# Optimization experiments

Hardware: AMD Instinct MI355X
Metric: run time of the kernel (lower is better)

## Reference

```python
import jax, jax.numpy as jnp
import numpy as np

BS, N, F, R, OUT = 8, 512, 512, 16, 512
ALPHA = 0.2

def setup_inputs() -> dict:
    key = jax.random.key(0)
    ks = jax.random.split(key, 16)
    w = lambda k, shp: (jax.random.normal(k, shp, dtype=jnp.float32) * 0.05)
    return {
        'x_ori': jax.random.normal(ks[0], (BS, N, F), dtype=jnp.float32),
        'x': jax.random.normal(ks[1], (BS, N, F), dtype=jnp.float32),
        'c': jax.random.normal(ks[2], (BS, 1, F), dtype=jnp.float32),
        'adj': jax.random.randint(ks[3], (BS, N, N, R), 0, 2, dtype=jnp.int32),
        'Wfc': w(ks[4], (F, F)),
        'Wdc': w(ks[5], (F, F)),
        'Wqv': w(ks[6], (2 * F, F)),
        'Wkv': w(ks[7], (2 * F, F)),
        'Wqc': w(ks[8], (F, F)),
        'Wkc': w(ks[9], (F, F)),
        'Wa': w(ks[10], (2 * F, R)),
        'Wu': w(ks[11], (2 * F, OUT)),
    }

def reference(x_ori, x, c, adj, Wfc, Wdc, Wqv, Wkv, Wqc, Wkc, Wa, Wu):
    # relation-context modulation vector m: [bs,1,F]
    m = jnp.matmul(jax.nn.elu(jnp.matmul(c, Wfc)), Wdc)
    nodes = jnp.concatenate([x, x_ori], axis=2)          # [bs,N,2F]
    xq = jnp.matmul(nodes, Wqv) * jnp.matmul(m, Wqc)     # [bs,N,F]
    xk = jnp.matmul(nodes, Wkv) * jnp.matmul(m, Wkc)     # [bs,N,F]
    # scores[b,i,j,r] = leakyrelu(xq_i . Wa[:F,r] + xk_j . Wa[F:,r])
    # (equivalent to cat([xq_i,xk_j]) @ Wa without materializing [bs,N,N,2F])
    sq = jnp.matmul(xq, Wa[:F])                          # [bs,N,R]
    sk = jnp.matmul(xk, Wa[F:])                          # [bs,N,R]
    scores = jax.nn.leaky_relu(sq[:, :, None, :] + sk[:, None, :, :], ALPHA)
    adj_f = adj.astype(scores.dtype)                     # [bs,N,N,R]
    s = jnp.sum(scores * adj_f, axis=3)                  # [bs,N,N]
    mask = jnp.sum(adj_f, axis=3) > 0
    attn = jax.nn.softmax(jnp.where(mask, s, jnp.float32(-9e15)), axis=2)
    new_x = jnp.matmul(attn, x)                          # [bs,N,F]
    return jnp.matmul(jnp.concatenate([x, new_x], axis=2), Wu)
```

## Files before the change

### kernel.cpp

```cpp
#include <hip/hip_runtime.h>
#include <hip/hip_bf16.h>
#include <cstddef>
#include <cstdint>

static constexpr int BSZ  = 8;
static constexpr int NN   = 512;
static constexpr int FF   = 512;
static constexpr int RR   = 16;
static constexpr int TWOF = 1024;

typedef __attribute__((ext_vector_type(8))) short short8;
typedef __attribute__((ext_vector_type(4))) float f32x4;

__device__ __forceinline__ ushort bf16_bits(float v) {
    union { __hip_bfloat16 h; ushort u; } cvt;
    cvt.h = __float2bfloat16(v);
    return cvt.u;
}

static constexpr size_t OFF_TB     = 0;
static constexpr size_t OFF_MB     = 16384;
static constexpr size_t OFF_MQ     = 32768;
static constexpr size_t OFF_MK     = 49152;
static constexpr size_t OFF_SQ     = 65536;
static constexpr size_t OFF_SK     = 327680;
static constexpr size_t OFF_WQET   = 589824;
static constexpr size_t OFF_WKET   = 851968;
static constexpr size_t OFF_XBF    = 5308416;
static constexpr size_t OFF_XTBF   = 9502720;
static constexpr size_t OFF_XORIBF = 13697024;
static constexpr size_t OFF_NEWXBF = 17891328;
static constexpr size_t OFF_WUT    = 22085632;
static constexpr size_t OFF_MASK   = 23134208;

__global__ __launch_bounds__(256) void k_prep(
    const float* __restrict__ x_ori, const float* __restrict__ x,
    const float* __restrict__ c, const float* __restrict__ Wfc,
    const float* __restrict__ Wu, const int* __restrict__ adj,
    ushort* __restrict__ xori_bf, ushort* __restrict__ x_bf,
    ushort* __restrict__ xT_bf, ushort* __restrict__ WuT,
    float* __restrict__ tb, ushort* __restrict__ masks)
{
    int blk = blockIdx.x;
    int t = threadIdx.x;
    if (blk < 1024) {
        int idx = blk * 256 + t;
        float4 a = ((const float4*)x_ori)[idx * 2];
        float4 b = ((const float4*)x_ori)[idx * 2 + 1];
        uint4 s;
        s.x = (uint)bf16_bits(a.x) | ((uint)bf16_bits(a.y) << 16);
        s.y = (uint)bf16_bits(a.z) | ((uint)bf16_bits(a.w) << 16);
        s.z = (uint)bf16_bits(b.x) | ((uint)bf16_bits(b.y) << 16);
        s.w = (uint)bf16_bits(b.z) | ((uint)bf16_bits(b.w) << 16);
        ((uint4*)xori_bf)[idx] = s;
    } else if (blk < 3072) {
        __shared__ float tile[32][33];
        int bb = blk - 1024;
        int f0 = (bb & 15) * 32, i0 = ((bb >> 4) & 15) * 32, b = bb >> 8;
        int c2 = (t & 15) * 2, r = t >> 4;
#pragma unroll
        for (int rr = 0; rr < 32; rr += 16) {
            int i = i0 + r + rr;
            const float* xp = &x[((size_t)b * NN + i) * FF + f0 + c2];
            float v0 = xp[0], v1 = xp[1];
            tile[r + rr][c2] = v0;
            tile[r + rr][c2 + 1] = v1;
            *(uint*)&x_bf[((size_t)b * NN + i) * FF + f0 + c2] =
                (uint)bf16_bits(v0) | ((uint)bf16_bits(v1) << 16);
        }
        __syncthreads();
#pragma unroll
        for (int ff = 0; ff < 32; ff += 16) {
            int f = f0 + r + ff;
            *(uint*)&xT_bf[((size_t)b * FF + f) * NN + i0 + c2] =
                (uint)bf16_bits(tile[c2][r + ff]) |
                ((uint)bf16_bits(tile[c2 + 1][r + ff]) << 16);
        }
    } else if (blk < 3584) {
        __shared__ float tile2[32][33];
        int bb = blk - 3072;
        int f0 = (bb & 31) * 32, o0 = (bb >> 5) * 32;
        int cc = t & 31, r0 = t >> 5;
#pragma unroll
        for (int rr = 0; rr < 32; rr += 8)
            tile2[r0 + rr][cc] = Wu[(size_t)(f0 + r0 + rr) * FF + o0 + cc];
        __syncthreads();
#pragma unroll
        for (int rr = 0; rr < 32; rr += 8)
            WuT[(size_t)(o0 + r0 + rr) * TWOF + f0 + cc] = bf16_bits(tile2[cc][r0 + rr]);
    } else if (blk < 3712) {
        __shared__ float red1[8][32];
        int bb = blk - 3584;
        int b = bb >> 4, f0 = (bb & 15) * 32;
        int f = t & 31, kq = t >> 5;
        const float* vb = c + (size_t)b * FF;
        float acc = 0.f;
        int ks = kq * 64;
#pragma unroll 8
        for (int k = ks; k < ks + 64; ++k)
            acc = fmaf(vb[k], Wfc[(size_t)k * FF + f0 + f], acc);
        red1[kq][f] = acc;
        __syncthreads();
        if (kq == 0) {
            acc += red1[1][f] + red1[2][f] + red1[3][f] + red1[4][f] +
                   red1[5][f] + red1[6][f] + red1[7][f];
            tb[(size_t)b * FF + f0 + f] = (acc > 0.f) ? acc : expm1f(acc);
        }
    } else {
        int idx = (blk - 3712) * 256 + t;
        const int4* ap = (const int4*)adj + (size_t)idx * 4;
        int4 a0 = ap[0], a1 = ap[1], a2 = ap[2], a3 = ap[3];
        uint m = 0;
        m |= (uint)a0.x;       m |= (uint)a0.y << 1;
        m |= (uint)a0.z << 2;  m |= (uint)a0.w << 3;
        m |= (uint)a1.x << 4;  m |= (uint)a1.y << 5;
        m |= (uint)a1.z << 6;  m |= (uint)a1.w << 7;
        m |= (uint)a2.x << 8;  m |= (uint)a2.y << 9;
        m |= (uint)a2.z << 10; m |= (uint)a2.w << 11;
        m |= (uint)a3.x << 12; m |= (uint)a3.y << 13;
        m |= (uint)a3.z << 14; m |= (uint)a3.w << 15;
        uint hi = (uint)__shfl_down((int)m, 1, 64);
        if (!(t & 1))
            ((uint*)masks)[idx >> 1] = m | (hi << 16);
    }
}

__global__ __launch_bounds__(256) void k_matvec(const float* __restrict__ vin,
                                                const float* __restrict__ W,
                                                float* __restrict__ vout) {
    __shared__ float red[8][32];
    int b = blockIdx.y;
    int f0 = blockIdx.x * 32;
    int t = threadIdx.x;
    int f = t & 31, kq = t >> 5;
    const float* vb = vin + (size_t)b * FF;
    float acc = 0.f;
    int ks = kq * 64;
#pragma unroll 8
    for (int k = ks; k < ks + 64; ++k)
        acc = fmaf(vb[k], W[(size_t)k * FF + f0 + f], acc);
    red[kq][f] = acc;
    __syncthreads();
    if (kq == 0) {
        acc += red[1][f] + red[2][f] + red[3][f] + red[4][f] +
               red[5][f] + red[6][f] + red[7][f];
        vout[(size_t)b * FF + f0 + f] = acc;
    }
}

__global__ __launch_bounds__(256) void k_mqk(const float* __restrict__ m,
                                             const float* __restrict__ Wqc,
                                             const float* __restrict__ Wkc,
                                             float* __restrict__ mq,
                                             float* __restrict__ mk) {
    __shared__ float redq[8][32];
    __shared__ float redk[8][32];
    int b = blockIdx.y;
    int f0 = blockIdx.x * 32;
    int t = threadIdx.x;
    int f = t & 31, kq = t >> 5;
    const float* mb = m + (size_t)b * FF;
    float aq = 0.f, ak = 0.f;
    int ks = kq * 64;
#pragma unroll 8
    for (int k = ks; k < ks + 64; ++k) {
        float mv = mb[k];
        aq = fmaf(mv, Wqc[(size_t)k * FF + f0 + f], aq);
        ak = fmaf(mv, Wkc[(size_t)k * FF + f0 + f], ak);
    }
    redq[kq][f] = aq;
    redk[kq][f] = ak;
    __syncthreads();
    if (kq == 0) {
        aq += redq[1][f] + redq[2][f] + redq[3][f] + redq[4][f] +
              redq[5][f] + redq[6][f] + redq[7][f];
        ak += redk[1][f] + redk[2][f] + redk[3][f] + redk[4][f] +
              redk[5][f] + redk[6][f] + redk[7][f];
        mq[(size_t)b * FF + f0 + f] = aq;
        mk[(size_t)b * FF + f0 + f] = ak;
    }
}

__global__ __launch_bounds__(256) void k_weff(const float* __restrict__ Wqv,
                                              const float* __restrict__ Wkv,
                                              const float* __restrict__ Wa,
                                              const float* __restrict__ mqv,
                                              const float* __restrict__ mkv,
                                              ushort* __restrict__ WqEt,
                                              ushort* __restrict__ WkEt) {
    int z = blockIdx.z;
    const float* W = z ? Wkv : Wqv;
    const float* mvec = z ? mkv : mqv;
    ushort* WeffT = z ? WkEt : WqEt;
    int waRowOff = z ? FF : 0;

    __shared__ float4 wa4[FF * 4];
    int tid = threadIdx.x;
    int b = blockIdx.y;
    const float* mv = mvec + (size_t)b * FF;
#pragma unroll
    for (int qq = 0; qq < 8; ++qq) {
        int idx = tid + qq * 256;
        int f = idx >> 2, rq = idx & 3;
        float4 w = *reinterpret_cast<const float4*>(Wa + (size_t)(waRowOff + f) * RR + rq * 4);
        float s = mv[f];
        float4 o;
        o.x = w.x * s; o.y = w.y * s; o.z = w.z * s; o.w = w.w * s;
        wa4[idx] = o;
    }
    __syncthreads();
    int k_l = tid >> 2, r4 = tid & 3;
    int k = blockIdx.x * 64 + k_l;
    const float4* Wrow4 = reinterpret_cast<const float4*>(W + (size_t)k * FF);
    float4 acc = {0.f, 0.f, 0.f, 0.f};
#pragma unroll 4
    for (int f4 = 0; f4 < FF / 4; ++f4) {
        float4 w = Wrow4[f4];
        float4 v0 = wa4[(f4 * 4 + 0) * 4 + r4];
        float4 v1 = wa4[(f4 * 4 + 1) * 4 + r4];
        float4 v2 = wa4[(f4 * 4 + 2) * 4 + r4];
        float4 v3 = wa4[(f4 * 4 + 3) * 4 + r4];
        acc.x = fmaf(w.x, v0.x, acc.x); acc.y = fmaf(w.x, v0.y, acc.y);
        acc.z = fmaf(w.x, v0.z, acc.z); acc.w = fmaf(w.x, v0.w, acc.w);
        acc.x = fmaf(w.y, v1.x, acc.x); acc.y = fmaf(w.y, v1.y, acc.y);
        acc.z = fmaf(w.y, v1.z, acc.z); acc.w = fmaf(w.y, v1.w, acc.w);
        acc.x = fmaf(w.z, v2.x, acc.x); acc.y = fmaf(w.z, v2.y, acc.y);
        acc.z = fmaf(w.z, v2.z, acc.z); acc.w = fmaf(w.z, v2.w, acc.w);
        acc.x = fmaf(w.w, v3.x, acc.x); acc.y = fmaf(w.w, v3.y, acc.y);
        acc.z = fmaf(w.w, v3.z, acc.z); acc.w = fmaf(w.w, v3.w, acc.w);
    }
    WeffT[((size_t)b * RR + r4 * 4 + 0) * TWOF + k] = bf16_bits(acc.x);
    WeffT[((size_t)b * RR + r4 * 4 + 1) * TWOF + k] = bf16_bits(acc.y);
    WeffT[((size_t)b * RR + r4 * 4 + 2) * TWOF + k] = bf16_bits(acc.z);
    WeffT[((size_t)b * RR + r4 * 4 + 3) * TWOF + k] = bf16_bits(acc.w);
}

__global__ __launch_bounds__(256) void k_sqsk(const ushort* __restrict__ x_bf,
                                              const ushort* __restrict__ xori_bf,
                                              const ushort* __restrict__ WqEt,
                                              const ushort* __restrict__ WkEt,
                                              float* __restrict__ sq,
                                              float* __restrict__ sk) {
    int t = threadIdx.x;
    int b = blockIdx.y;
    int m0 = blockIdx.x * 32;
    int lane = t & 63, w = t >> 6;
    int sub = w & 1, isK = w >> 1;
    int m_l = lane & 15, q = lane >> 4;
    int row = m0 + sub * 16 + m_l;
    const ushort* Bt = (isK ? WkEt : WqEt) + ((size_t)b * RR + m_l) * TWOF;
    f32x4 acc = {0.f, 0.f, 0.f, 0.f};
#pragma unroll
    for (int k0 = 0; k0 < TWOF; k0 += 32) {
        const ushort* src = (k0 < FF) ? x_bf : xori_bf;
        int kc = k0 & (FF - 1);
        short8 af = *(const short8*)(src + ((size_t)b * NN + row) * FF + kc + q * 8);
        short8 bf = *(const short8*)(Bt + k0 + q * 8);
        acc = __builtin_amdgcn_mfma_f32_16x16x32_bf16(af, bf, acc, 0, 0, 0);
    }
    float* dst = isK ? sk : sq;
#pragma unroll
    for (int r = 0; r < 4; ++r) {
        int i = m0 + sub * 16 + q * 4 + r;
        dst[((size_t)b * NN + i) * RR + m_l] = acc[r];
    }
}

__global__ __launch_bounds__(256) void k_attn_pv(const ushort* __restrict__ masks,
                                                 const float* __restrict__ sq,
                                                 const float* __restrict__ sk,
                                                 const ushort* __restrict__ xT_bf,
                                                 ushort* __restrict__ newx_bf) {
    constexpr int ZS = 520;
    __shared__ float  zbuf[8 * ZS];
    __shared__ ushort P[16 * ZS];
    __shared__ ushort mask_lds[8 * NN];
    __shared__ float  rowsum[8];
    int t = threadIdx.x;
    int b = blockIdx.y;
    int m0 = blockIdx.x * 8;

    {
        const uint4* mg = (const uint4*)(masks + ((size_t)b * NN + m0) * NN);
        uint4* ml = (uint4*)mask_lds;
        ml[t] = mg[t];
        ml[t + 256] = mg[t + 256];
    }
    __syncthreads();

    {
        int r = t >> 5, cc = t & 31;
        int i = m0 + r;
        const float4* sqp = (const float4*)(sq + ((size_t)b * NN + i) * RR);
        float4 q0 = sqp[0], q1 = sqp[1], q2 = sqp[2], q3 = sqp[3];
        float sv[16] = {q0.x, q0.y, q0.z, q0.w, q1.x, q1.y, q1.z, q1.w,
                        q2.x, q2.y, q2.z, q2.w, q3.x, q3.y, q3.z, q3.w};
#pragma unroll 4
        for (int it = 0; it < 16; ++it) {
            int j = it * 32 + cc;
            uint mk = mask_lds[r * NN + j];
            const float4* kp = (const float4*)(sk + ((size_t)b * NN + j) * RR);
            float4 s0 = kp[0], s1 = kp[1], s2 = kp[2], s3 = kp[3];
            float ssum = 0.f;
#define LR_TERM(SVAL, RIDX)                                         \
            { float v_ = sv[RIDX] + (SVAL);                         \
              v_ = fmaxf(v_, 0.2f * v_);                            \
              ssum = fmaf(v_, (float)((mk >> RIDX) & 1u), ssum); }
            LR_TERM(s0.x, 0)  LR_TERM(s0.y, 1)
            LR_TERM(s0.z, 2)  LR_TERM(s0.w, 3)
            LR_TERM(s1.x, 4)  LR_TERM(s1.y, 5)
            LR_TERM(s1.z, 6)  LR_TERM(s1.w, 7)
            LR_TERM(s2.x, 8)  LR_TERM(s2.y, 9)
            LR_TERM(s2.z, 10) LR_TERM(s2.w, 11)
            LR_TERM(s3.x, 12) LR_TERM(s3.y, 13)
            LR_TERM(s3.z, 14) LR_TERM(s3.w, 15)
#undef LR_TERM
            zbuf[r * ZS + j] = mk ? ssum : -9e15f;
        }
    }
    __syncthreads();

    {
        uint* pz = (uint*)&P[8 * ZS];
#pragma unroll
        for (int idx = t; idx < (8 * ZS) / 2; idx += 256) pz[idx] = 0u;

        int w = t >> 6, lane = t & 63;
        int rr = w * 2 + (lane >> 5);
        int cc = lane & 31;
        const float* zr = &zbuf[rr * ZS];
        float mx = -3.0e38f;
#pragma unroll
        for (int it = 0; it < 16; ++it) mx = fmaxf(mx, zr[it * 32 + cc]);
#pragma unroll
        for (int off = 1; off < 32; off <<= 1) mx = fmaxf(mx, __shfl_xor(mx, off, 64));
        float sum = 0.f;
        ushort* pr = &P[rr * ZS];
#pragma unroll
        for (int it = 0; it < 16; ++it) {
            float e = __expf(zr[it * 32 + cc] - mx);
            pr[it * 32 + cc] = bf16_bits(e);
            sum += e;
        }
#pragma unroll
        for (int off = 1; off < 32; off <<= 1) sum += __shfl_xor(sum, off, 64);
        if (cc == 0) rowsum[rr] = sum;
    }
    __syncthreads();

    {
        int w = t >> 6, lane = t & 63;
        int m_l = lane & 15, q = lane >> 4;
        int n0w = w * 128;
        f32x4 acc[8] = {};
        const ushort* xTb = xT_bf + (size_t)b * FF * NN;
        for (int k0 = 0; k0 < NN; k0 += 32) {
            short8 af = *(const short8*)(&P[m_l * ZS + k0 + q * 8]);
#pragma unroll
            for (int nb = 0; nb < 8; ++nb) {
                int n = n0w + nb * 16 + m_l;
                short8 bfr = *(const short8*)(xTb + (size_t)n * NN + k0 + q * 8);
                acc[nb] = __builtin_amdgcn_mfma_f32_16x16x32_bf16(af, bfr, acc[nb], 0, 0, 0);
            }
        }
        if (q < 2) {
            float inv[4];
#pragma unroll
            for (int rg = 0; rg < 4; ++rg) inv[rg] = 1.f / rowsum[q * 4 + rg];
#pragma unroll
            for (int nb = 0; nb < 8; ++nb) {
#pragma unroll
                for (int rg = 0; rg < 4; ++rg) {
                    int i = m0 + q * 4 + rg;
                    int f = n0w + nb * 16 + m_l;
                    newx_bf[((size_t)b * NN + i) * FF + f] = bf16_bits(acc[nb][rg] * inv[rg]);
                }
            }
        }
    }
}

__global__ __launch_bounds__(256) void k_gemm(const ushort* __restrict__ A1, size_t sA1,
                                              const ushort* __restrict__ A2, size_t sA2,
                                              const ushort* __restrict__ BT, size_t sBT,
                                              float* __restrict__ Cf, size_t sC,
                                              int K, int ldBT) {
    __shared__ ushort As[2][64 * 40];
    __shared__ ushort Bs[2][64 * 40];
    int t = threadIdx.x;
    int n0 = blockIdx.x * 64, m0 = blockIdx.y * 64, b = blockIdx.z;
    int row = t >> 2, c8 = (t & 3) * 8;
    int lane = t & 63, w = t >> 6;
    int m_l = lane & 15, q = lane >> 4;
    f32x4 acc[4] = {{0.f,0.f,0.f,0.f},{0.f,0.f,0.f,0.f},{0.f,0.f,0.f,0.f},{0.f,0.f,0.f,0.f}};
    const ushort* BTb = BT + (size_t)b * sBT;
    for (int k0 = 0; k0 < K; k0 += 64) {
#pragma unroll
        for (int h = 0; h < 2; ++h) {
            int kk = k0 + h * 32;
            const ushort* Aab; int kc;
            if (kk < FF) { Aab = A1 + (size_t)b * sA1; kc = kk; }
            else         { Aab = A2 + (size_t)b * sA2; kc = kk - FF; }
            uint4 av = *(const uint4*)(Aab + (size_t)(m0 + row) * FF + kc + c8);
            uint4 bv = *(const uint4*)(BTb + (size_t)(n0 + row) * ldBT + kk + c8);
            *(uint4*)(&As[h][row * 40 + c8]) = av;
            *(uint4*)(&Bs[h][row * 40 + c8]) = bv;
        }
        __syncthreads();
#pragma unroll
        for (int h = 0; h < 2; ++h) {
            short8 af = *(const short8*)(&As[h][(w * 16 + m_l) * 40 + q * 8]);
#pragma unroll
            for (int nb = 0; nb < 4; ++nb) {
                short8 bfr = *(const short8*)(&Bs[h][(nb * 16 + m_l) * 40 + q * 8]);
                acc[nb] = __builtin_amdgcn_mfma_f32_16x16x32_bf16(af, bfr, acc[nb], 0, 0, 0);
            }
        }
        __syncthreads();
    }
#pragma unroll
    for (int nb = 0; nb < 4; ++nb) {
#pragma unroll
        for (int r = 0; r < 4; ++r) {
            int mi = m0 + w * 16 + q * 4 + r;
            int ni = n0 + nb * 16 + m_l;
            Cf[(size_t)b * sC + (size_t)mi * FF + ni] = acc[nb][r];
        }
    }
}

extern "C" void kernel_launch(void* const* d_in, const int* in_sizes, int n_in,
                              void* d_out, int out_size, void* d_ws, size_t ws_size,
                              hipStream_t stream) {
    const float* x_ori = (const float*)d_in[0];
    const float* x     = (const float*)d_in[1];
    const float* c     = (const float*)d_in[2];
    const int*   adj   = (const int*)d_in[3];
    const float* Wfc   = (const float*)d_in[4];
    const float* Wdc   = (const float*)d_in[5];
    const float* Wqv   = (const float*)d_in[6];
    const float* Wkv   = (const float*)d_in[7];
    const float* Wqc   = (const float*)d_in[8];
    const float* Wkc   = (const float*)d_in[9];
    const float* Wa    = (const float*)d_in[10];
    const float* Wu    = (const float*)d_in[11];
    float* out = (float*)d_out;

    char* ws = (char*)d_ws;
    float*  tb      = (float*)(ws + OFF_TB);
    float*  mb      = (float*)(ws + OFF_MB);
    float*  mq      = (float*)(ws + OFF_MQ);
    float*  mk      = (float*)(ws + OFF_MK);
    float*  sq      = (float*)(ws + OFF_SQ);
    float*  sk      = (float*)(ws + OFF_SK);
    ushort* WqEt    = (ushort*)(ws + OFF_WQET);
    ushort* WkEt    = (ushort*)(ws + OFF_WKET);
    ushort* x_bf    = (ushort*)(ws + OFF_XBF);
    ushort* xT_bf   = (ushort*)(ws + OFF_XTBF);
    ushort* xori_bf = (ushort*)(ws + OFF_XORIBF);
    ushort* newx_bf = (ushort*)(ws + OFF_NEWXBF);
    ushort* WuT     = (ushort*)(ws + OFF_WUT);
    ushort* masks   = (ushort*)(ws + OFF_MASK);

    dim3 blk(256);

    k_prep<<<dim3(11904), blk, 0, stream>>>(x_ori, x, c, Wfc, Wu, adj,
                                            xori_bf, x_bf, xT_bf, WuT, tb, masks);

    k_matvec<<<dim3(16, BSZ), blk, 0, stream>>>(tb, Wdc, mb);
    k_mqk<<<dim3(16, BSZ), blk, 0, stream>>>(mb, Wqc, Wkc, mq, mk);

    k_weff<<<dim3(16, BSZ, 2), blk, 0, stream>>>(Wqv, Wkv, Wa, mq, mk, WqEt, WkEt);

    k_sqsk<<<dim3(16, BSZ), blk, 0, stream>>>(x_bf, xori_bf, WqEt, WkEt, sq, sk);

    k_attn_pv<<<dim3(64, BSZ), blk, 0, stream>>>(masks, sq, sk, xT_bf, newx_bf);

    k_gemm<<<dim3(8, 8, BSZ), blk, 0, stream>>>(
        x_bf, (size_t)NN * FF, newx_bf, (size_t)NN * FF,
        WuT, (size_t)0, out, (size_t)NN * FF, TWOF, TWOF);
}
```

Before: 322.2 us.

## Coalesce adjacency mask packing and stage transposed sk in LDS for attention

The adjacency packing path now has each thread read one int4 per iteration over 16 iterations. This makes consecutive lanes read consecutive 16-byte chunks, and the 16-bit relation masks are assembled with xor shuffles, so the grid shrinks from 11904 to 5760 blocks. In the attention kernel, sk for the batch is loaded once into LDS transposed by relation. Scores are kept in registers and the softmax is fused into the score pass, which removes the zbuf round trip and one barrier. The costs are more LDS (32 KB for sk_t), a launch-bounds hint of 2 blocks per CU, and more register pressure from the z array.

```diff
diff --git a/kernel.cpp b/kernel.cpp
--- a/kernel.cpp
+++ b/kernel.cpp
@@ -107,21 +107,21 @@
             tb[(size_t)b * FF + f0 + f] = (acc > 0.f) ? acc : expm1f(acc);
         }
     } else {
-        int idx = (blk - 3712) * 256 + t;
-        const int4* ap = (const int4*)adj + (size_t)idx * 4;
-        int4 a0 = ap[0], a1 = ap[1], a2 = ap[2], a3 = ap[3];
-        uint m = 0;
-        m |= (uint)a0.x;       m |= (uint)a0.y << 1;
-        m |= (uint)a0.z << 2;  m |= (uint)a0.w << 3;
-        m |= (uint)a1.x << 4;  m |= (uint)a1.y << 5;
-        m |= (uint)a1.z << 6;  m |= (uint)a1.w << 7;
-        m |= (uint)a2.x << 8;  m |= (uint)a2.y << 9;
-        m |= (uint)a2.z << 10; m |= (uint)a2.w << 11;
-        m |= (uint)a3.x << 12; m |= (uint)a3.y << 13;
-        m |= (uint)a3.z << 14; m |= (uint)a3.w << 15;
-        uint hi = (uint)__shfl_down((int)m, 1, 64);
-        if (!(t & 1))
-            ((uint*)masks)[idx >> 1] = m | (hi << 16);
+        int pb = (blk - 3712) * 1024;
+        const int4* a4 = (const int4*)adj;
+        uint* m32 = (uint*)masks;
+#pragma unroll 8
+        for (int i = 0; i < 16; ++i) {
+            size_t g4 = (size_t)pb * 4 + (size_t)i * 256 + t;
+            int4 v = a4[g4];
+            uint bits = (uint)v.x | ((uint)v.y << 1) | ((uint)v.z << 2) | ((uint)v.w << 3);
+            uint mp = bits << ((t & 3) * 4);
+            mp |= (uint)__shfl_xor((int)mp, 1, 64);
+            mp |= (uint)__shfl_xor((int)mp, 2, 64);
+            uint hi = (uint)__shfl_xor((int)mp, 4, 64);
+            if ((t & 7) == 0)
+                m32[(size_t)pb / 2 + i * 32 + (t >> 3)] = (mp & 0xFFFFu) | (hi << 16);
+        }
     }
 }
 
@@ -266,14 +266,14 @@
     }
 }
 
-__global__ __launch_bounds__(256) void k_attn_pv(const ushort* __restrict__ masks,
-                                                 const float* __restrict__ sq,
-                                                 const float* __restrict__ sk,
-                                                 const ushort* __restrict__ xT_bf,
-                                                 ushort* __restrict__ newx_bf) {
+__global__ __launch_bounds__(256, 2) void k_attn_pv(const ushort* __restrict__ masks,
+                                                    const float* __restrict__ sq,
+                                                    const float* __restrict__ sk,
+                                                    const ushort* __restrict__ xT_bf,
+                                                    ushort* __restrict__ newx_bf) {
     constexpr int ZS = 520;
-    __shared__ float  zbuf[8 * ZS];
     __shared__ ushort P[16 * ZS];
+    __shared__ float  sk_t[16 * NN];
     __shared__ ushort mask_lds[8 * NN];
     __shared__ float  rowsum[8];
     int t = threadIdx.x;
@@ -285,6 +285,19 @@
         uint4* ml = (uint4*)mask_lds;
         ml[t] = mg[t];
         ml[t + 256] = mg[t + 256];
+        const float4* skg = (const float4*)(sk + (size_t)b * NN * RR);
+#pragma unroll
+        for (int qq = 0; qq < 8; ++qq) {
+            int idx = t + qq * 256;
+            float4 v = skg[idx];
+            int j = idx >> 2, rr = (idx & 3) * 4;
+            sk_t[(rr + 0) * NN + j] = v.x;
+            sk_t[(rr + 1) * NN + j] = v.y;
+            sk_t[(rr + 2) * NN + j] = v.z;
+            sk_t[(rr + 3) * NN + j] = v.w;
+        }
+        uint* pz = (uint*)&P[8 * ZS];
+        for (int idx = t; idx < (8 * ZS) / 2; idx += 256) pz[idx] = 0u;
     }
     __syncthreads();
 
@@ -295,56 +308,36 @@
         float4 q0 = sqp[0], q1 = sqp[1], q2 = sqp[2], q3 = sqp[3];
         float sv[16] = {q0.x, q0.y, q0.z, q0.w, q1.x, q1.y, q1.z, q1.w,
                         q2.x, q2.y, q2.z, q2.w, q3.x, q3.y, q3.z, q3.w};
-#pragma unroll 4
+        float z[16];
+#pragma unroll
         for (int it = 0; it < 16; ++it) {
             int j = it * 32 + cc;
             uint mk = mask_lds[r * NN + j];
-            const float4* kp = (const float4*)(sk + ((size_t)b * NN + j) * RR);
-            float4 s0 = kp[0], s1 = kp[1], s2 = kp[2], s3 = kp[3];
             float ssum = 0.f;
-#define LR_TERM(SVAL, RIDX)                                         \
-            { float v_ = sv[RIDX] + (SVAL);                         \
-              v_ = fmaxf(v_, 0.2f * v_);                            \
-              ssum = fmaf(v_, (float)((mk >> RIDX) & 1u), ssum); }
-            LR_TERM(s0.x, 0)  LR_TERM(s0.y, 1)
-            LR_TERM(s0.z, 2)  LR_TERM(s0.w, 3)
-            LR_TERM(s1.x, 4)  LR_TERM(s1.y, 5)
-            LR_TERM(s1.z, 6)  LR_TERM(s1.w, 7)
-            LR_TERM(s2.x, 8)  LR_TERM(s2.y, 9)
-            LR_TERM(s2.z, 10) LR_TERM(s2.w, 11)
-            LR_TERM(s3.x, 12) LR_TERM(s3.y, 13)
-            LR_TERM(s3.z, 14) LR_TERM(s3.w, 15)
-#undef LR_TERM
-            zbuf[r * ZS + j] = mk ? ssum : -9e15f;
-        }
-    }
-    __syncthreads();
-
-    {
-        uint* pz = (uint*)&P[8 * ZS];
-#pragma unroll
-        for (int idx = t; idx < (8 * ZS) / 2; idx += 256) pz[idx] = 0u;
-
-        int w = t >> 6, lane = t & 63;
-        int rr = w * 2 + (lane >> 5);
-        int cc = lane & 31;
-        const float* zr = &zbuf[rr * ZS];
-        float mx = -3.0e38f;
-#pragma unroll
-        for (int it = 0; it < 16; ++it) mx = fmaxf(mx, zr[it * 32 + cc]);
-#pragma unroll
-        for (int off = 1; off < 32; off <<= 1) mx = fmaxf(mx, __shfl_xor(mx, off, 64));
+#pragma unroll
+            for (int ridx = 0; ridx < 16; ++ridx) {
+                float v_ = sv[ridx] + sk_t[ridx * NN + j];
+                v_ = fmaxf(v_, 0.2f * v_);
+                ssum = fmaf(v_, (float)((mk >> ridx) & 1u), ssum);
+            }
+            z[it] = mk ? ssum : -9e15f;
+        }
+        float mx = z[0];
+#pragma unroll
+        for (int it = 1; it < 16; ++it) mx = fmaxf(mx, z[it]);
+#pragma unroll
+        for (int off = 1; off < 32; off <<= 1) mx = fmaxf(mx, __shfl_xor(mx, off, 32));
         float sum = 0.f;
-        ushort* pr = &P[rr * ZS];
+        ushort* pr = &P[r * ZS];
 #pragma unroll
         for (int it = 0; it < 16; ++it) {
-            float e = __expf(zr[it * 32 + cc] - mx);
+            float e = __expf(z[it] - mx);
             pr[it * 32 + cc] = bf16_bits(e);
             sum += e;
         }
 #pragma unroll
-        for (int off = 1; off < 32; off <<= 1) sum += __shfl_xor(sum, off, 64);
-        if (cc == 0) rowsum[rr] = sum;
+        for (int off = 1; off < 32; off <<= 1) sum += __shfl_xor(sum, off, 32);
+        if (cc == 0) rowsum[r] = sum;
     }
     __syncthreads();
 
@@ -464,8 +457,8 @@
 
     dim3 blk(256);
 
-    k_prep<<<dim3(11904), blk, 0, stream>>>(x_ori, x, c, Wfc, Wu, adj,
-                                            xori_bf, x_bf, xT_bf, WuT, tb, masks);
+    k_prep<<<dim3(5760), blk, 0, stream>>>(x_ori, x, c, Wfc, Wu, adj,
+                                           xori_bf, x_bf, xT_bf, WuT, tb, masks);
 
     k_matvec<<<dim3(16, BSZ), blk, 0, stream>>>(tb, Wdc, mb);
     k_mqk<<<dim3(16, BSZ), blk, 0, stream>>>(mb, Wqc, Wkc, mq, mk);
```

Result: no change. 327.8 us (+1.7%).
